# Kernel optimization log

Measured on AMD Instinct MI355X. Metric: run time of the kernel, lower is better.

Reference implementation:

```python
import jax, jax.numpy as jnp
import numpy as np

B, L, D = 16384, 5, 1024  # batch, lesionNum, feat_dim == att_dim
LN_EPS = 1e-5


def _layernorm(x, g, b):
    mu = jnp.mean(x, axis=-1, keepdims=True)
    var = jnp.var(x, axis=-1, keepdims=True)
    return (x - mu) * jax.lax.rsqrt(var + LN_EPS) * g + b


def setup_inputs() -> dict:
    key = jax.random.key(0)
    ks = jax.random.split(key, 8)
    s = 0.02
    x = jax.random.normal(ks[0], (B, L, D), dtype=jnp.float32)
    mask = jax.random.randint(ks[1], (1, L), 0, 2, dtype=jnp.int64)
    mask = mask.at[0, 0].set(1)  # guarantee at least one unmasked position
    Wq = jax.random.normal(ks[2], (D, D), dtype=jnp.float32) * s
    Wk = jax.random.normal(ks[3], (D, D), dtype=jnp.float32) * s
    Wv = jax.random.normal(ks[4], (D, D), dtype=jnp.float32) * s
    W1 = jax.random.normal(ks[5], (D, D), dtype=jnp.float32) * s
    b1 = jnp.zeros((D,), dtype=jnp.float32)
    W2 = jax.random.normal(ks[6], (D, D), dtype=jnp.float32) * s
    b2 = jnp.zeros((D,), dtype=jnp.float32)
    att_g = jnp.ones((D,), dtype=jnp.float32)
    att_b = jnp.zeros((D,), dtype=jnp.float32)
    ff_g = jnp.ones((D,), dtype=jnp.float32)
    ff_b = jnp.zeros((D,), dtype=jnp.float32)
    return dict(x=x, mask=mask, Wq=Wq, Wk=Wk, Wv=Wv, W1=W1, b1=b1, W2=W2,
                b2=b2, att_g=att_g, att_b=att_b, ff_g=ff_g, ff_b=ff_b)


def reference(x, mask, Wq, Wk, Wv, W1, b1, W2, b2, att_g, att_b, ff_g, ff_b):
    # QKV (no bias). With nhead=1 the reshape makes scores per-token dot
    # products: (B,L,1,D) @ (B,L,D,1) -> (B,L,1,1); we keep them as (B,L).
    q = jnp.einsum('bld,ed->ble', x, Wq)
    k = jnp.einsum('bld,ed->ble', x, Wk)
    v = jnp.einsum('bld,ed->ble', x, Wv)
    scores = jnp.sum(q * k, axis=-1) / jnp.sqrt(jnp.float32(D))  # (B,L)
    # torch loop sets -inf where ANY mask row has 0 (applied to all batches)
    keep = jnp.all(mask != 0, axis=0)  # (L,)
    scores = jnp.where(keep[None, :], scores, -jnp.inf)
    probs = jax.nn.softmax(scores, axis=1)  # softmax over token dim (dim=1)
    probs = jnp.where(jnp.isnan(probs), 0.0, probs)  # nan-safe (all-masked)
    attn = probs[:, :, None] * v  # (B,L,1,1)@(B,L,1,D) == per-token scaling
    y = _layernorm(attn + x, att_g, att_b)
    # FFN: Linear -> exact GELU -> Linear (dropout inactive in eval)
    h = jax.nn.gelu(jnp.einsum('bld,ed->ble', y, W1) + b1, approximate=False)
    ff = jnp.einsum('bld,ed->ble', h, W2) + b2
    return _layernorm(ff + y, ff_g, ff_b)
```

## Files before the change

### kernel.cpp

```cpp
#include <hip/hip_runtime.h>
#include <hip/hip_bf16.h>
#include <cstdint>


typedef float f32x4 __attribute__((ext_vector_type(4)));
typedef __bf16 bf16x8 __attribute__((ext_vector_type(8)));

#define DD 1024
#define NROWS 81920L

__device__ __forceinline__ unsigned short f2bf(float f) {
  union { float f; unsigned u; } c; c.f = f;
  unsigned u = c.u;
  return (unsigned short)((u + 0x7FFFu + ((u >> 16) & 1u)) >> 16);
}
__device__ __forceinline__ float bf2f(unsigned short b) {
  union { unsigned u; float f; } c; c.u = ((unsigned)b) << 16;
  return c.f;
}
__device__ __forceinline__ void unpack8(uint4 v, float* o) {
  o[0] = bf2f((unsigned short)(v.x & 0xffffu)); o[1] = bf2f((unsigned short)(v.x >> 16));
  o[2] = bf2f((unsigned short)(v.y & 0xffffu)); o[3] = bf2f((unsigned short)(v.y >> 16));
  o[4] = bf2f((unsigned short)(v.z & 0xffffu)); o[5] = bf2f((unsigned short)(v.z >> 16));
  o[6] = bf2f((unsigned short)(v.w & 0xffffu)); o[7] = bf2f((unsigned short)(v.w >> 16));
}
__device__ __forceinline__ void gload_lds16(const void* g, void* l) {
  __builtin_amdgcn_global_load_lds(
      (const __attribute__((address_space(1))) unsigned int*)g,
      (__attribute__((address_space(3))) unsigned int*)l, 16, 0, 0);
}

__global__ void __launch_bounds__(256) k_cvt_bf16(const float* __restrict__ in,
                                                  unsigned short* __restrict__ out, long n) {
  long i = ((long)blockIdx.x * blockDim.x + threadIdx.x) * 8;
  long stride = (long)gridDim.x * blockDim.x * 8;
  for (; i < n; i += stride) {
    f32x4 a = *(const f32x4*)(in + i);
    f32x4 b = *(const f32x4*)(in + i + 4);
    uint4 o;
    o.x = (unsigned)f2bf(a[0]) | ((unsigned)f2bf(a[1]) << 16);
    o.y = (unsigned)f2bf(a[2]) | ((unsigned)f2bf(a[3]) << 16);
    o.z = (unsigned)f2bf(b[0]) | ((unsigned)f2bf(b[1]) << 16);
    o.w = (unsigned)f2bf(b[2]) | ((unsigned)f2bf(b[3]) << 16);
    *(uint4*)(out + i) = o;
  }
}

__global__ void __launch_bounds__(256) k_gt(const float* __restrict__ Wq,
                                            const float* __restrict__ Wk,
                                            unsigned short* __restrict__ Gt) {
  __shared__ float sk[16][16];
  __shared__ float sq[16][64];
  const int tx = threadIdx.x, ty = threadIdx.y;
  const int n0 = blockIdx.y * 16;
  const int k0 = blockIdx.x * 64;
  float acc[4] = {0.f, 0.f, 0.f, 0.f};
  for (int e0 = 0; e0 < 1024; e0 += 16) {
    sk[ty][tx] = Wk[(long)(e0 + ty) * DD + n0 + tx];
    *(f32x4*)&sq[ty][tx * 4] = *(const f32x4*)&Wq[(long)(e0 + ty) * DD + k0 + tx * 4];
    __syncthreads();
#pragma unroll
    for (int ee = 0; ee < 16; ++ee) {
      float kv = sk[ee][ty];
      f32x4 qv = *(const f32x4*)&sq[ee][tx * 4];
      acc[0] += kv * qv[0]; acc[1] += kv * qv[1];
      acc[2] += kv * qv[2]; acc[3] += kv * qv[3];
    }
    __syncthreads();
  }
  uint2 o;
  o.x = (unsigned)f2bf(acc[0]) | ((unsigned)f2bf(acc[1]) << 16);
  o.y = (unsigned)f2bf(acc[2]) | ((unsigned)f2bf(acc[3]) << 16);
  *(uint2*)&Gt[(long)(n0 + ty) * DD + k0 + tx * 4] = o;
}

#define VMBAR(N)                                             \
  do {                                                       \
    asm volatile("s_waitcnt vmcnt(" #N ")" ::: "memory");    \
    __builtin_amdgcn_s_barrier();                            \
    asm volatile("" ::: "memory");                           \
  } while (0)

template <int EPI>
__global__ void __launch_bounds__(512, 2) k_gemm256(
    const unsigned short* __restrict__ A,
    const unsigned short* __restrict__ B,
    unsigned short* __restrict__ outb,
    float* __restrict__ outf,
    const float* __restrict__ bias,
    const unsigned short* __restrict__ resid,
    const int ntl2,
    const int cst) {
  __shared__ __align__(16) char ldsB[131072];
  const int tid = threadIdx.x;
  const int lane = tid & 63;
  const int wid = tid >> 6;
  const int wm = wid >> 2, wn = wid & 3;

  const int nwg = gridDim.x;
  const int cpx = nwg >> 3;
  const int d = blockIdx.x;
  const int l = (d & 7) * cpx + (d >> 3);
  const int mt = l >> ntl2;
  const int nt = l & ((1 << ntl2) - 1);
  const long m0 = (long)mt * 256;
  const int n0 = nt * 256;

  const int r0off = tid * 16;
  const int r1off = 8192 + tid * 16;
  const int rw0 = r0off >> 6, rw1 = r1off >> 6;
  const int oc0 = (r0off & 63) ^ (((rw0 >> 1) & 3) << 4);
  const int oc1 = (r1off & 63) ^ (((rw1 >> 1) & 3) << 4);
  const char* sA0 = (const char*)A + (m0 + rw0) * 2048 + oc0;
  const char* sA1 = (const char*)A + (m0 + rw1) * 2048 + oc1;
  const char* sB0 = (const char*)B + (long)(n0 + rw0) * 2048 + oc0;
  const char* sB1 = (const char*)B + (long)(n0 + rw1) * 2048 + oc1;

  const int la = lane & 15, lg = lane >> 4;
  const int cb = ((lg ^ ((la >> 1) & 3)) << 4);
  int aoff[8], boff[4];
#pragma unroll
  for (int mi = 0; mi < 8; ++mi) aoff[mi] = (wm * 128 + mi * 16 + la) * 64 + cb;
#pragma unroll
  for (int nj = 0; nj < 4; ++nj) boff[nj] = (wn * 64 + nj * 16 + la) * 64 + cb;

  f32x4 acc[8][4];
#pragma unroll
  for (int mi = 0; mi < 8; ++mi)
#pragma unroll
    for (int nj = 0; nj < 4; ++nj) acc[mi][nj] = f32x4{0.f, 0.f, 0.f, 0.f};

  auto stage = [&](int kt) {
    char* base = ldsB + ((kt & 3) << 15);
    const long ko = (long)kt << 6;
    gload_lds16(sA0 + ko, base + r0off);
    gload_lds16(sA1 + ko, base + r1off);
    gload_lds16(sB0 + ko, base + 16384 + r0off);
    gload_lds16(sB1 + ko, base + 16384 + r1off);
  };

  auto body = [&](int kt) {
    const char* bA = ldsB + ((kt & 3) << 15);
    const char* bB = bA + 16384;
    bf16x8 fb[4];
#pragma unroll
    for (int nj = 0; nj < 4; ++nj) fb[nj] = *(const bf16x8*)(bB + boff[nj]);
    __builtin_amdgcn_s_setprio(1);
#pragma unroll
    for (int mi = 0; mi < 8; ++mi) {
      bf16x8 a = *(const bf16x8*)(bA + aoff[mi]);
#pragma unroll
      for (int nj = 0; nj < 4; ++nj)
        acc[mi][nj] = __builtin_amdgcn_mfma_f32_16x16x32_bf16(a, fb[nj], acc[mi][nj], 0, 0, 0);
    }
    __builtin_amdgcn_s_setprio(0);
    __builtin_amdgcn_s_barrier();
    asm volatile("" ::: "memory");
  };

  stage(0); stage(1); stage(2);
  for (int kt = 0; kt < 29; ++kt) {
    stage(kt + 3);
    VMBAR(12);
    body(kt);
  }
  VMBAR(8);  body(29);
  VMBAR(4);  body(30);
  VMBAR(0);  body(31);

  const long rbase = m0 + wm * 128 + (lane >> 4) * 4;
  const int cbase = n0 + wn * 64 + la;
#pragma unroll
  for (int mi = 0; mi < 8; ++mi) {
#pragma unroll
    for (int nj = 0; nj < 4; ++nj) {
      const int col = cbase + nj * 16;
      float bv = 0.f;
      if constexpr (EPI != 0) bv = bias[col];
#pragma unroll
      for (int t = 0; t < 4; ++t) {
        const long r = rbase + mi * 16 + t;
        float v = acc[mi][nj][t];
        if constexpr (EPI == 0) {
          outb[r * (long)cst + col] = f2bf(v);
        } else if constexpr (EPI == 1) {
          v += bv;
          v = 0.5f * v * (1.0f + erff(v * 0.70710678118654752f));
          outb[r * (long)cst + col] = f2bf(v);
        } else {
          v += bv + bf2f(resid[r * (long)cst + col]);
          outf[r * (long)cst + col] = v;
        }
      }
    }
  }
}

__global__ void __launch_bounds__(256) k_attn_ln(
    const unsigned short* __restrict__ xb, const unsigned short* __restrict__ uv,
    unsigned short* __restrict__ yb, const int* __restrict__ mask,
    const float* __restrict__ att_g, const float* __restrict__ att_b) {
  const int b = blockIdx.x * 4 + (threadIdx.x >> 6);
  const int lane = threadIdx.x & 63;
  const long xbase = (long)b * 5120 + lane * 16;
  const long ubase = (long)b * 10240 + lane * 16;

  float xr[5][16];
  float sc[5];
#pragma unroll
  for (int l = 0; l < 5; ++l) {
    const unsigned short* xp = xb + xbase + l * 1024;
    const unsigned short* up = uv + ubase + l * 2048;
    unpack8(*(const uint4*)xp, xr[l]); unpack8(*(const uint4*)(xp + 8), xr[l] + 8);
    float uu[16];
    unpack8(*(const uint4*)up, uu); unpack8(*(const uint4*)(up + 8), uu + 8);
    float d = 0.f;
#pragma unroll
    for (int c = 0; c < 16; ++c) d += xr[l][c] * uu[c];
#pragma unroll
    for (int off = 32; off; off >>= 1) d += __shfl_xor(d, off);
    sc[l] = d * 0.03125f;
  }
  bool keep[5];
  float m = -1e30f;
#pragma unroll
  for (int l = 0; l < 5; ++l) {
    keep[l] = (mask[l] != 0);
    if (keep[l]) m = fmaxf(m, sc[l]);
  }
  float p[5], s = 0.f;
#pragma unroll
  for (int l = 0; l < 5; ++l) {
    p[l] = keep[l] ? __expf(sc[l] - m) : 0.f;
    s += p[l];
  }
  const float inv = 1.f / s;

  float gg[16], bb[16];
  {
    const float* gp = att_g + lane * 16;
    const float* bp = att_b + lane * 16;
#pragma unroll
    for (int q = 0; q < 4; ++q) {
      f32x4 gv = *(const f32x4*)(gp + q * 4);
      f32x4 bv = *(const f32x4*)(bp + q * 4);
#pragma unroll
      for (int c = 0; c < 4; ++c) { gg[q * 4 + c] = gv[c]; bb[q * 4 + c] = bv[c]; }
    }
  }

#pragma unroll
  for (int l = 0; l < 5; ++l) {
    const unsigned short* vp = uv + ubase + l * 2048 + 1024;
    float vv[16];
    unpack8(*(const uint4*)vp, vv); unpack8(*(const uint4*)(vp + 8), vv + 8);
    const float pl = p[l] * inv;
    float t[16], sm = 0.f, sq = 0.f;
#pragma unroll
    for (int c = 0; c < 16; ++c) {
      t[c] = pl * vv[c] + xr[l][c];
      sm += t[c];
      sq += t[c] * t[c];
    }
#pragma unroll
    for (int off = 32; off; off >>= 1) {
      sm += __shfl_xor(sm, off);
      sq += __shfl_xor(sq, off);
    }
    const float mu = sm * (1.f / 1024.f);
    const float var = sq * (1.f / 1024.f) - mu * mu;
    const float rs = rsqrtf(var + 1e-5f);
    unsigned short r[16];
#pragma unroll
    for (int c = 0; c < 16; ++c) r[c] = f2bf((t[c] - mu) * rs * gg[c] + bb[c]);
    uint4 o0, o1;
    o0.x = (unsigned)r[0] | ((unsigned)r[1] << 16);  o0.y = (unsigned)r[2] | ((unsigned)r[3] << 16);
    o0.z = (unsigned)r[4] | ((unsigned)r[5] << 16);  o0.w = (unsigned)r[6] | ((unsigned)r[7] << 16);
    o1.x = (unsigned)r[8] | ((unsigned)r[9] << 16);  o1.y = (unsigned)r[10] | ((unsigned)r[11] << 16);
    o1.z = (unsigned)r[12] | ((unsigned)r[13] << 16); o1.w = (unsigned)r[14] | ((unsigned)r[15] << 16);
    unsigned short* yp = yb + xbase + l * 1024;
    *(uint4*)yp = o0;
    *(uint4*)(yp + 8) = o1;
  }
}

__global__ void __launch_bounds__(256) k_ln_final(float* __restrict__ z,
                                                  const float* __restrict__ g,
                                                  const float* __restrict__ bb) {
  const int lane = threadIdx.x & 63;
  const long row = (long)blockIdx.x * 4 + (threadIdx.x >> 6);
  float* p = z + row * DD + lane * 16;
  f32x4 v[4];
  float sm = 0.f, sq = 0.f;
#pragma unroll
  for (int q = 0; q < 4; ++q) {
    v[q] = *(const f32x4*)(p + q * 4);
#pragma unroll
    for (int c = 0; c < 4; ++c) { sm += v[q][c]; sq += v[q][c] * v[q][c]; }
  }
#pragma unroll
  for (int off = 32; off; off >>= 1) {
    sm += __shfl_xor(sm, off);
    sq += __shfl_xor(sq, off);
  }
  const float mu = sm * (1.f / 1024.f);
  const float var = sq * (1.f / 1024.f) - mu * mu;
  const float rs = rsqrtf(var + 1e-5f);
  const float* gp = g + lane * 16;
  const float* bp = bb + lane * 16;
#pragma unroll
  for (int q = 0; q < 4; ++q) {
    f32x4 gv = *(const f32x4*)(gp + q * 4);
    f32x4 bv = *(const f32x4*)(bp + q * 4);
#pragma unroll
    for (int c = 0; c < 4; ++c) v[q][c] = (v[q][c] - mu) * rs * gv[c] + bv[c];
    *(f32x4*)(p + q * 4) = v[q];
  }
}

extern "C" void kernel_launch(void* const* d_in, const int* in_sizes, int n_in,
                              void* d_out, int out_size, void* d_ws, size_t ws_size,
                              hipStream_t stream) {
  const float* x     = (const float*)d_in[0];
  const int*   mask  = (const int*)d_in[1];
  const float* Wq    = (const float*)d_in[2];
  const float* Wk    = (const float*)d_in[3];
  const float* Wv    = (const float*)d_in[4];
  const float* W1    = (const float*)d_in[5];
  const float* b1    = (const float*)d_in[6];
  const float* W2    = (const float*)d_in[7];
  const float* b2    = (const float*)d_in[8];
  const float* att_g = (const float*)d_in[9];
  const float* att_b = (const float*)d_in[10];
  const float* ff_g  = (const float*)d_in[11];
  const float* ff_b  = (const float*)d_in[12];

  const long NE = NROWS * DD;
  unsigned short* xb   = (unsigned short*)d_ws;
  unsigned short* hb   = xb + NE;
  unsigned short* Bcat = hb + NE;
  unsigned short* W1b  = Bcat + 2L * DD * DD;
  unsigned short* W2b  = W1b + (long)DD * DD;

  unsigned short* uvb = (unsigned short*)d_out;
  float* outf = (float*)d_out;

  k_cvt_bf16<<<2048, 256, 0, stream>>>(x, xb, NE);
  k_cvt_bf16<<<512, 256, 0, stream>>>(Wv, Bcat + (long)DD * DD, (long)DD * DD);
  k_cvt_bf16<<<512, 256, 0, stream>>>(W1, W1b, (long)DD * DD);
  k_cvt_bf16<<<512, 256, 0, stream>>>(W2, W2b, (long)DD * DD);
  k_gt<<<dim3(16, 64), dim3(16, 16), 0, stream>>>(Wq, Wk, Bcat);

  k_gemm256<0><<<2560, 512, 0, stream>>>(xb, Bcat, uvb, nullptr, nullptr, nullptr, 3, 2048);
  k_attn_ln<<<4096, 256, 0, stream>>>(xb, uvb, xb, mask, att_g, att_b);
  k_gemm256<1><<<1280, 512, 0, stream>>>(xb, W1b, hb, nullptr, b1, nullptr, 2, 1024);
  k_gemm256<2><<<1280, 512, 0, stream>>>(hb, W2b, nullptr, outf, b2, xb, 2, 1024);
  k_ln_final<<<20480, 256, 0, stream>>>(outf, ff_g, ff_b);
}
```

Before: 1.350 ms.

## Split GEMM k-tile into two half-phases interleaving loads with MFMA; bf16 intermediate for final LN

The GEMM main loop now splits each k-tile into two halves. A-tile global-to-LDS loads are issued during the first half and B-tile loads during the second, with explicit barriers, lgkmcnt waits and sched_barriers, so memory traffic overlaps MFMA work and register pressure drops. A new epilogue variant writes the second FFN GEMM's residual sum as bf16 into workspace, read by a new bf16-input final LayerNorm kernel, which halves that intermediate's write and read traffic. This adds barriers per tile and costs some precision in the pre-LN values. The bf16 path is taken only when the workspace is large enough.

```diff
diff --git a/kernel.cpp b/kernel.cpp
--- a/kernel.cpp
+++ b/kernel.cpp
@@ -130,43 +130,64 @@
 #pragma unroll
     for (int nj = 0; nj < 4; ++nj) acc[mi][nj] = f32x4{0.f, 0.f, 0.f, 0.f};
 
-  auto stage = [&](int kt) {
+  auto stageA = [&](int kt) {
     char* base = ldsB + ((kt & 3) << 15);
     const long ko = (long)kt << 6;
     gload_lds16(sA0 + ko, base + r0off);
     gload_lds16(sA1 + ko, base + r1off);
-    gload_lds16(sB0 + ko, base + 16384 + r0off);
-    gload_lds16(sB1 + ko, base + 16384 + r1off);
   };
-
-  auto body = [&](int kt) {
+  auto stageB = [&](int kt) {
+    char* base = ldsB + ((kt & 3) << 15) + 16384;
+    const long ko = (long)kt << 6;
+    gload_lds16(sB0 + ko, base + r0off);
+    gload_lds16(sB1 + ko, base + r1off);
+  };
+
+  auto tile = [&](int kt, bool st) {
     const char* bA = ldsB + ((kt & 3) << 15);
     const char* bB = bA + 16384;
-    bf16x8 fb[4];
-#pragma unroll
-    for (int nj = 0; nj < 4; ++nj) fb[nj] = *(const bf16x8*)(bB + boff[nj]);
+    bf16x8 fa[4], fb[4];
+#pragma unroll
+    for (int i = 0; i < 4; ++i) fa[i] = *(const bf16x8*)(bA + aoff[i]);
+#pragma unroll
+    for (int j = 0; j < 4; ++j) fb[j] = *(const bf16x8*)(bB + boff[j]);
+    if (st) stageA(kt + 3);
+    __builtin_amdgcn_s_barrier();
+    asm volatile("s_waitcnt lgkmcnt(0)" ::: "memory");
+    __builtin_amdgcn_sched_barrier(0);
     __builtin_amdgcn_s_setprio(1);
 #pragma unroll
-    for (int mi = 0; mi < 8; ++mi) {
-      bf16x8 a = *(const bf16x8*)(bA + aoff[mi]);
-#pragma unroll
-      for (int nj = 0; nj < 4; ++nj)
-        acc[mi][nj] = __builtin_amdgcn_mfma_f32_16x16x32_bf16(a, fb[nj], acc[mi][nj], 0, 0, 0);
-    }
+    for (int i = 0; i < 4; ++i)
+#pragma unroll
+      for (int j = 0; j < 4; ++j)
+        acc[i][j] = __builtin_amdgcn_mfma_f32_16x16x32_bf16(fa[i], fb[j], acc[i][j], 0, 0, 0);
     __builtin_amdgcn_s_setprio(0);
     __builtin_amdgcn_s_barrier();
-    asm volatile("" ::: "memory");
+#pragma unroll
+    for (int i = 0; i < 4; ++i) fa[i] = *(const bf16x8*)(bA + aoff[4 + i]);
+    if (st) stageB(kt + 3);
+    __builtin_amdgcn_s_barrier();
+    asm volatile("s_waitcnt lgkmcnt(0)" ::: "memory");
+    __builtin_amdgcn_sched_barrier(0);
+    __builtin_amdgcn_s_setprio(1);
+#pragma unroll
+    for (int i = 0; i < 4; ++i)
+#pragma unroll
+      for (int j = 0; j < 4; ++j)
+        acc[4 + i][j] = __builtin_amdgcn_mfma_f32_16x16x32_bf16(fa[i], fb[j], acc[4 + i][j], 0, 0, 0);
+    __builtin_amdgcn_s_setprio(0);
   };
 
-  stage(0); stage(1); stage(2);
+  stageA(0); stageB(0); stageA(1); stageB(1); stageA(2); stageB(2);
+  VMBAR(8);
+
   for (int kt = 0; kt < 29; ++kt) {
-    stage(kt + 3);
-    VMBAR(12);
-    body(kt);
-  }
-  VMBAR(8);  body(29);
-  VMBAR(4);  body(30);
-  VMBAR(0);  body(31);
+    tile(kt, true);
+    VMBAR(8);
+  }
+  tile(29, false); VMBAR(4);
+  tile(30, false); VMBAR(0);
+  tile(31, false);
 
   const long rbase = m0 + wm * 128 + (lane >> 4) * 4;
   const int cbase = n0 + wn * 64 + la;
@@ -187,9 +208,12 @@
           v += bv;
           v = 0.5f * v * (1.0f + erff(v * 0.70710678118654752f));
           outb[r * (long)cst + col] = f2bf(v);
+        } else if constexpr (EPI == 2) {
+          v += bv + bf2f(resid[r * (long)cst + col]);
+          outf[r * (long)cst + col] = v;
         } else {
           v += bv + bf2f(resid[r * (long)cst + col]);
-          outf[r * (long)cst + col] = v;
+          outb[r * (long)cst + col] = f2bf(v);
         }
       }
     }
@@ -315,6 +339,41 @@
 #pragma unroll
     for (int c = 0; c < 4; ++c) v[q][c] = (v[q][c] - mu) * rs * gv[c] + bv[c];
     *(f32x4*)(p + q * 4) = v[q];
+  }
+}
+
+__global__ void __launch_bounds__(256) k_ln_final_bf(const unsigned short* __restrict__ zb,
+                                                     float* __restrict__ out,
+                                                     const float* __restrict__ g,
+                                                     const float* __restrict__ bb) {
+  const int lane = threadIdx.x & 63;
+  const long row = (long)blockIdx.x * 4 + (threadIdx.x >> 6);
+  const unsigned short* p = zb + row * DD + lane * 16;
+  float t[16];
+  unpack8(*(const uint4*)p, t);
+  unpack8(*(const uint4*)(p + 8), t + 8);
+  float sm = 0.f, sq = 0.f;
+#pragma unroll
+  for (int c = 0; c < 16; ++c) { sm += t[c]; sq += t[c] * t[c]; }
+#pragma unroll
+  for (int off = 32; off; off >>= 1) {
+    sm += __shfl_xor(sm, off);
+    sq += __shfl_xor(sq, off);
+  }
+  const float mu = sm * (1.f / 1024.f);
+  const float var = sq * (1.f / 1024.f) - mu * mu;
+  const float rs = rsqrtf(var + 1e-5f);
+  float* op = out + row * DD + lane * 16;
+  const float* gp = g + lane * 16;
+  const float* bp = bb + lane * 16;
+#pragma unroll
+  for (int q = 0; q < 4; ++q) {
+    f32x4 gv = *(const f32x4*)(gp + q * 4);
+    f32x4 bv = *(const f32x4*)(bp + q * 4);
+    f32x4 o;
+#pragma unroll
+    for (int c = 0; c < 4; ++c) o[c] = (t[q * 4 + c] - mu) * rs * gv[c] + bv[c];
+    *(f32x4*)(op + q * 4) = o;
   }
 }
 
@@ -341,6 +400,10 @@
   unsigned short* Bcat = hb + NE;
   unsigned short* W1b  = Bcat + 2L * DD * DD;
   unsigned short* W2b  = W1b + (long)DD * DD;
+  unsigned short* zb   = W2b + (long)DD * DD;
+
+  const size_t need_zb = (size_t)(3L * NE + 4L * DD * DD) * 2;
+  const bool use_zb = ws_size >= need_zb;
 
   unsigned short* uvb = (unsigned short*)d_out;
   float* outf = (float*)d_out;
@@ -354,6 +417,11 @@
   k_gemm256<0><<<2560, 512, 0, stream>>>(xb, Bcat, uvb, nullptr, nullptr, nullptr, 3, 2048);
   k_attn_ln<<<4096, 256, 0, stream>>>(xb, uvb, xb, mask, att_g, att_b);
   k_gemm256<1><<<1280, 512, 0, stream>>>(xb, W1b, hb, nullptr, b1, nullptr, 2, 1024);
-  k_gemm256<2><<<1280, 512, 0, stream>>>(hb, W2b, nullptr, outf, b2, xb, 2, 1024);
-  k_ln_final<<<20480, 256, 0, stream>>>(outf, ff_g, ff_b);
-}
+  if (use_zb) {
+    k_gemm256<3><<<1280, 512, 0, stream>>>(hb, W2b, zb, nullptr, b2, xb, 2, 1024);
+    k_ln_final_bf<<<20480, 256, 0, stream>>>(zb, outf, ff_g, ff_b);
+  } else {
+    k_gemm256<2><<<1280, 512, 0, stream>>>(hb, W2b, nullptr, outf, b2, xb, 2, 1024);
+    k_ln_final<<<20480, 256, 0, stream>>>(outf, ff_g, ff_b);
+  }
+}
```

After: 1.269 ms. -5.9%, faster.
